# Optimization experiments

Measured on AMD Instinct MI355X. Metric: run time of the kernel, lower is better.

The kernel has to match this reference:

```python
import jax, jax.numpy as jnp
import numpy as np

N = 50000      # nodes
E = 800000     # edges (avg degree 16)
NF = 128       # input feature dim
H = 128        # hidden dim
GAMMA = 1.0    # gm init arg
COS_EPS = 1e-8 # F.cosine_similarity eps
EW_MIN = 1e-4  # edge-weight clamp


def setup_inputs() -> dict:
    key = jax.random.key(0)
    ks = jax.random.split(key, 9)
    x = jax.random.normal(ks[0], (N, NF), dtype=jnp.float32)
    edge_index = jax.random.randint(ks[1], (2, E), 0, N, dtype=jnp.int64)
    sensitive_attr = jax.random.randint(ks[2], (N,), 0, 2, dtype=jnp.int64)
    s1 = 1.0 / np.sqrt(NF)
    s2 = 1.0 / np.sqrt(H)
    W1 = jax.random.normal(ks[3], (NF, H), dtype=jnp.float32) * s1
    b1 = jnp.zeros((H,), dtype=jnp.float32)
    W2 = jax.random.normal(ks[4], (H, H), dtype=jnp.float32) * s2
    b2 = jnp.zeros((H,), dtype=jnp.float32)
    Wc = jax.random.normal(ks[5], (H, 1), dtype=jnp.float32) * s2
    bc = jnp.zeros((1,), dtype=jnp.float32)
    return {"x": x, "edge_index": edge_index, "sensitive_attr": sensitive_attr,
            "W1": W1, "b1": b1, "W2": W2, "b2": b2, "Wc": Wc, "bc": bc}


def gcn_conv(x, W, b, src, dst, ew, n):
    """PyG GCNConv: lin -> symmetric-normalized edge-weighted aggregation (+self loops) -> bias."""
    xt = x @ W                                              # [N,H]
    deg = jax.ops.segment_sum(ew, dst, num_segments=n) + 1.0  # self-loop weight 1
    dinv = jnp.where(deg > 0, deg ** -0.5, 0.0)             # [N]
    norm = dinv[src] * ew * dinv[dst]                       # [E]
    agg = jax.ops.segment_sum(xt[src] * norm[:, None], dst, num_segments=n)
    # self-loop contribution: norm_ii = dinv[i] * 1 * dinv[i]
    return agg + xt * (dinv * dinv)[:, None] + b


def reference(x, edge_index, sensitive_attr, W1, b1, W2, b2, Wc, bc):
    src, dst = edge_index[0], edge_index[1]
    # cosine-similarity edge weights (gather-heavy)
    xs, xd = x[src], x[dst]                                  # [E,F] each
    dot = jnp.sum(xs * xd, axis=1)
    ns = jnp.maximum(jnp.sqrt(jnp.sum(xs * xs, axis=1)), COS_EPS)
    nd = jnp.maximum(jnp.sqrt(jnp.sum(xd * xd, axis=1)), COS_EPS)
    sim = dot / (ns * nd)
    sen_diff = (sensitive_attr[src] != sensitive_attr[dst]).astype(x.dtype)
    ew = jnp.maximum(sim * jnp.exp(-GAMMA * sen_diff), EW_MIN)
    # two GCN layers (dropout is identity in eval mode)
    h = jax.nn.relu(gcn_conv(x, W1, b1, src, dst, ew, N))
    h = jax.nn.relu(gcn_conv(h, W2, b2, src, dst, ew, N))
    y = h @ Wc + bc                                          # [N,1]
    return (y, h)
```

## Files before the change

kernel.cpp:

```cpp
#include <hip/hip_runtime.h>


typedef unsigned short u16;
typedef unsigned int u32;
typedef __attribute__((ext_vector_type(8))) short short8;
typedef __attribute__((ext_vector_type(4))) float floatx4;

__device__ __forceinline__ float bflo(u32 u){ return __uint_as_float(u << 16); }
__device__ __forceinline__ float bfhi(u32 u){ return __uint_as_float(u & 0xFFFF0000u); }
__device__ __forceinline__ float bf1(u16 u){ return __uint_as_float(((u32)u) << 16); }
__device__ __forceinline__ u16 f2bf(float f){
    u32 u = __float_as_uint(f);
    u += 0x7FFFu + ((u >> 16) & 1u);
    return (u16)(u >> 16);
}
__device__ __forceinline__ u32 pack2(float a, float b){
    return (u32)f2bf(a) | ((u32)f2bf(b) << 16);
}
__device__ __forceinline__ float wsum(float v){
#pragma unroll
    for (int o = 32; o > 0; o >>= 1) v += __shfl_xor(v, o, 64);
    return v;
}
__device__ __forceinline__ float ld1(const void* p, size_t idx, int f32){
    return f32 ? ((const float*)p)[idx] : bf1(((const u16*)p)[idx]);
}
__device__ __forceinline__ int ldidx(const int* p, size_t i, int i64){
    return i64 ? p[2 * i] : p[i];
}

__global__ void classify_k(const u32* __restrict__ xw, const int* __restrict__ eiw,
                           int* __restrict__ flags, int* __restrict__ bcnt)
{
    __shared__ int c_out, c_nz;
    int t = threadIdx.x;
    if (t == 0) { c_out = 0; c_nz = 0; }
    if (t < 256) bcnt[t] = 0;
    __syncthreads();
    u32 w = xw[t];
    int e = (w >> 7) & 0xFF;
    int outl = (e < 110 || e > 140) ? 1 : 0;
    int nz = (eiw[2 * t + 1] != 0) ? 1 : 0;
    atomicAdd(&c_out, outl);
    atomicAdd(&c_nz, nz);
    __syncthreads();
    if (t == 0) { flags[0] = (c_out > 256); flags[1] = (c_nz < 256); }
}

__global__ __launch_bounds__(256) void convhist_k(const void* __restrict__ x,
                                                  u32* __restrict__ xb,
                                                  float* __restrict__ rn, int N,
                                                  const int* __restrict__ ei,
                                                  const int* __restrict__ sa,
                                                  int* __restrict__ bcnt, int E,
                                                  const void* __restrict__ W1,
                                                  const void* __restrict__ W2,
                                                  uint4* __restrict__ wf1,
                                                  uint4* __restrict__ wf2,
                                                  const int* __restrict__ flags,
                                                  int nbN, int nbH)
{
    __shared__ int lb[256];
    int b = blockIdx.x;
    if (b < nbN) {
        int i = b * 4 + (threadIdx.x >> 6);
        if (i >= N) return;
        int lane = threadIdx.x & 63;
        u32 u;
        if (flags[0]) {
            const float* q = (const float*)x + (size_t)i * 128 + lane * 2;
            u = pack2(q[0], q[1]);
        } else u = ((const u32*)x)[(size_t)i * 64 + lane];
        xb[(size_t)i * 64 + lane] = u;
        float f0 = bflo(u), f1 = bfhi(u);
        float ss = wsum(f0 * f0 + f1 * f1);
        if (lane == 0) {
            float r = 1.0f / fmaxf(sqrtf(ss), 1e-8f);
            int a = flags[1] ? sa[2 * (size_t)i] : sa[i];
            rn[i] = a ? -r : r;
        }
    } else if (b < nbN + nbH) {
        int t = threadIdx.x;
        lb[t] = 0;
        __syncthreads();
        int i64 = flags[1];
        size_t base = (size_t)(b - nbN) * 8192;
#pragma unroll 4
        for (int k = 0; k < 32; ++k) {
            size_t e = base + (size_t)k * 256 + t;
            if (e < (size_t)E) {
                int d = ldidx(ei, (size_t)E + e, i64);
                if ((u32)d >= (u32)N) d = 0;
                atomicAdd(&lb[d >> 8], 1);
            }
        }
        __syncthreads();
        int c = lb[t];
        if (c) atomicAdd(&bcnt[t], c);
    } else {
        int slot = (b - nbN - nbH) * 256 + threadIdx.x;
        if (slot >= 4096) return;
        int f32w = flags[0];
        const void* W = (slot < 2048) ? W1 : W2;
        uint4* wf = (slot < 2048) ? wf1 : wf2;
        int s = slot & 2047;
        int lane = s & 63, kk = (s >> 6) & 3, ct = s >> 8;
        int q = lane >> 4, n = lane & 15;
        int col = ct * 16 + n, k0 = kk * 32 + q * 8;
        union { u16 us[8]; uint4 u4; } tmp;
#pragma unroll
        for (int j = 0; j < 8; ++j)
            tmp.us[j] = f2bf(ld1(W, (size_t)(k0 + j) * 128 + col, f32w));
        wf[s] = tmp.u4;
    }
}

__global__ void bscan_k(const int* __restrict__ bcnt, int* __restrict__ bbase,
                        int* __restrict__ bcur, int* __restrict__ rowp, int N)
{
    int lane = threadIdx.x;
    int carry = 0;
    for (int base = 0; base < 256; base += 64) {
        int i = base + lane;
        int v = bcnt[i];
        int sc = v;
#pragma unroll
        for (int o = 1; o < 64; o <<= 1) {
            int nv = __shfl_up(sc, o);
            if (lane >= o) sc += nv;
        }
        int excl = carry + sc - v;
        bbase[i] = excl;
        bcur[i] = excl;
        carry += __shfl(sc, 63);
    }
    if (lane == 0) { bbase[256] = carry; rowp[N] = carry; }
}

__global__ __launch_bounds__(256) void bucket_k(const int* __restrict__ ei,
                                                int* __restrict__ bcur,
                                                u32* __restrict__ tmp,
                                                int E, int N,
                                                const int* __restrict__ flags)
{
    __shared__ int lh[256];
    __shared__ int gb[256];
    int t = threadIdx.x;
    lh[t] = 0;
    __syncthreads();
    int i64 = flags[1];
    size_t base = (size_t)blockIdx.x * 4096;
    u32 pay[16], meta[16];
#pragma unroll
    for (int k = 0; k < 16; ++k) {
        size_t e = base + (size_t)k * 256 + t;
        if (e < (size_t)E) {
            int s = ldidx(ei, e, i64);
            int d = ldidx(ei, (size_t)E + e, i64);
            if ((u32)s >= (u32)N) s = 0;
            if ((u32)d >= (u32)N) d = 0;
            int b = d >> 8;
            pay[k] = ((u32)s << 8) | ((u32)d & 0xFFu);
            int r = atomicAdd(&lh[b], 1);
            meta[k] = ((u32)r << 8) | (u32)b;
        } else meta[k] = 0xFFFFFFFFu;
    }
    __syncthreads();
    int c = lh[t];
    gb[t] = c ? atomicAdd(&bcur[t], c) : 0;
    __syncthreads();
#pragma unroll
    for (int k = 0; k < 16; ++k) {
        if (meta[k] != 0xFFFFFFFFu) {
            int b = (int)(meta[k] & 0xFFu);
            int r = (int)(meta[k] >> 8);
            tmp[gb[b] + r] = pay[k];
        }
    }
}

__global__ __launch_bounds__(256) void scat2_k(const int* __restrict__ bbase,
                                               int* __restrict__ rowp,
                                               const u32* __restrict__ tmp,
                                               u32* __restrict__ rec,
                                               int N, int E)
{
    __shared__ int lcnt[256];
    __shared__ int wtot[4];
    int b = blockIdx.x, t = threadIdx.x;
    int lane = t & 63, w = t >> 6;
    int n0 = b << 8;
    int p0 = bbase[b], p1 = bbase[b + 1];
    if (p0 < 0) p0 = 0;
    if (p1 > E) p1 = E;
    lcnt[t] = 0;
    __syncthreads();
    for (int idx = p0 + t; idx < p1; idx += 256)
        atomicAdd(&lcnt[tmp[idx] & 0xFFu], 1);
    __syncthreads();
    int v = lcnt[t];
    int sc = v;
#pragma unroll
    for (int o = 1; o < 64; o <<= 1) {
        int nv = __shfl_up(sc, o);
        if (lane >= o) sc += nv;
    }
    if (lane == 63) wtot[w] = sc;
    __syncthreads();
    int wo = 0;
#pragma unroll
    for (int k = 0; k < 4; ++k) { int s = wtot[k]; if (k < w) wo += s; }
    int excl = wo + sc - v;
    int node = n0 + t;
    if (node < N) rowp[node] = p0 + excl;
    lcnt[t] = excl;
    __syncthreads();
    for (int idx = p0 + t; idx < p1; idx += 256) {
        u32 pay = tmp[idx];
        int r = atomicAdd(&lcnt[pay & 0xFFu], 1);
        int pos = p0 + r;
        if ((u32)pos >= (u32)E) pos = 0;
        rec[pos] = pay >> 8;
    }
}

__global__ __launch_bounds__(256) void ewcsr_k(const u32* __restrict__ xb,
                                               const float* __restrict__ rn,
                                               const int* __restrict__ rowp,
                                               u32* __restrict__ rec,
                                               float* __restrict__ dv,
                                               int N, int E)
{
    int i = blockIdx.x * 4 + (threadIdx.x >> 6);
    if (i >= N) return;
    int lane = threadIdx.x & 63, g = lane >> 4, j = lane & 15;
    uint4 D = ((const uint4*)(xb + (size_t)i * 64))[j];
    float rni = rn[i];
    int p0 = rowp[i], p1 = rowp[i + 1];
    if (p0 < 0) p0 = 0;
    if (p1 > E) p1 = E;
    float acc = 0.0f;
    int p = p0 + g;
    for (; p + 4 < p1; p += 8) {
        int s0 = (int)rec[p];     if ((u32)s0 >= (u32)N) s0 = 0;
        int s1 = (int)rec[p + 4]; if ((u32)s1 >= (u32)N) s1 = 0;
        uint4 A0 = ((const uint4*)(xb + (size_t)s0 * 64))[j];
        uint4 A1 = ((const uint4*)(xb + (size_t)s1 * 64))[j];
        float d0 = bflo(A0.x) * bflo(D.x) + bfhi(A0.x) * bfhi(D.x)
                 + bflo(A0.y) * bflo(D.y) + bfhi(A0.y) * bfhi(D.y)
                 + bflo(A0.z) * bflo(D.z) + bfhi(A0.z) * bfhi(D.z)
                 + bflo(A0.w) * bflo(D.w) + bfhi(A0.w) * bfhi(D.w);
        float d1 = bflo(A1.x) * bflo(D.x) + bfhi(A1.x) * bfhi(D.x)
                 + bflo(A1.y) * bflo(D.y) + bfhi(A1.y) * bfhi(D.y)
                 + bflo(A1.z) * bflo(D.z) + bfhi(A1.z) * bfhi(D.z)
                 + bflo(A1.w) * bflo(D.w) + bfhi(A1.w) * bfhi(D.w);
#pragma unroll
        for (int o = 8; o > 0; o >>= 1) {
            d0 += __shfl_xor(d0, o);
            d1 += __shfl_xor(d1, o);
        }
        if (j == 0) {
            float pr0 = rn[s0] * rni;
            float w0 = fmaxf(d0 * fabsf(pr0) *
                             ((pr0 < 0.0f) ? 0.36787944117144233f : 1.0f), 1e-4f);
            u16 wb0 = f2bf(w0);
            rec[p] = ((u32)s0 << 16) | wb0;
            acc += bf1(wb0);
            float pr1 = rn[s1] * rni;
            float w1 = fmaxf(d1 * fabsf(pr1) *
                             ((pr1 < 0.0f) ? 0.36787944117144233f : 1.0f), 1e-4f);
            u16 wb1 = f2bf(w1);
            rec[p + 4] = ((u32)s1 << 16) | wb1;
            acc += bf1(wb1);
        }
    }
    if (p < p1) {
        int s0 = (int)rec[p]; if ((u32)s0 >= (u32)N) s0 = 0;
        uint4 A0 = ((const uint4*)(xb + (size_t)s0 * 64))[j];
        float d0 = bflo(A0.x) * bflo(D.x) + bfhi(A0.x) * bfhi(D.x)
                 + bflo(A0.y) * bflo(D.y) + bfhi(A0.y) * bfhi(D.y)
                 + bflo(A0.z) * bflo(D.z) + bfhi(A0.z) * bfhi(D.z)
                 + bflo(A0.w) * bflo(D.w) + bfhi(A0.w) * bfhi(D.w);
#pragma unroll
        for (int o = 8; o > 0; o >>= 1) d0 += __shfl_xor(d0, o);
        if (j == 0) {
            float pr0 = rn[s0] * rni;
            float w0 = fmaxf(d0 * fabsf(pr0) *
                             ((pr0 < 0.0f) ? 0.36787944117144233f : 1.0f), 1e-4f);
            u16 wb0 = f2bf(w0);
            rec[p] = ((u32)s0 << 16) | wb0;
            acc += bf1(wb0);
        }
    }
    acc += __shfl_xor(acc, 16);
    acc += __shfl_xor(acc, 32);
    if (lane == 0) dv[i] = 1.0f / sqrtf(1.0f + acc);
}

__global__ __launch_bounds__(256) void aggemm_k(const u32* __restrict__ feat,
                                                const int* __restrict__ rowp,
                                                const u32* __restrict__ rec,
                                                const float* __restrict__ dinv,
                                                const uint4* __restrict__ wfrag,
                                                const void* __restrict__ bias,
                                                void* __restrict__ out, int outbf,
                                                int N, int E,
                                                const void* __restrict__ Wc,
                                                const void* __restrict__ bc,
                                                float* __restrict__ yout,
                                                const int* __restrict__ flags)
{
    __shared__ float Acc[4][16][132];
    int t = threadIdx.x, wave = t >> 6, lane = t & 63;
    int rowbase = blockIdx.x * 64 + wave * 16;

    int idx = rowbase + lane;
    int rbreg = E;
    if (lane < 17) {
        int ii = idx < N ? idx : N;
        int v = rowp[ii];
        rbreg = v < 0 ? 0 : (v > E ? E : v);
    }
    float dreg = 0.0f;
    if (lane < 16 && idx < N) dreg = dinv[idx];

    for (int r = 0; r < 16; ++r) {
        int i = rowbase + r;
        float s0 = 0.0f, s1 = 0.0f;
        if (i < N) {
            float di = __shfl(dreg, r), sc = di * di;
            u32 u = feat[(size_t)i * 64 + lane];
            s0 = bflo(u) * sc; s1 = bfhi(u) * sc;
        }
        float2 st; st.x = s0; st.y = s1;
        *(float2*)&Acc[wave][r][2 * lane] = st;
    }

    int P0 = __shfl(rbreg, 0), P16 = __shfl(rbreg, 16);
    int crow = 0;
    int nb = __shfl(rbreg, 1);
    float dic = __shfl(dreg, 0);
    float a0 = 0.0f, a1 = 0.0f;
    int p = P0;
    for (; p + 15 < P16; p += 16) {
        u32 rr[16]; int s[16]; u32 v[16]; float dvs[16];
#pragma unroll
        for (int k = 0; k < 16; ++k) {
            rr[k] = rec[p + k];
            s[k] = rr[k] >> 16;
            if (s[k] >= N) s[k] = 0;
        }
#pragma unroll
        for (int k = 0; k < 16; ++k) v[k] = feat[(size_t)s[k] * 64 + lane];
#pragma unroll
        for (int k = 0; k < 16; ++k) dvs[k] = dinv[s[k]];
#pragma unroll
        for (int k = 0; k < 16; ++k) {
            int e = p + k;
            if (e >= nb) {
                float2* ap = (float2*)&Acc[wave][crow][2 * lane];
                float2 cv = *ap; cv.x += a0; cv.y += a1; *ap = cv;
                do { ++crow; nb = __shfl(rbreg, crow + 1); } while (e >= nb);
                dic = __shfl(dreg, crow & 15);
                a0 = 0.0f; a1 = 0.0f;
            }
            float w = bf1((u16)rr[k]) * dic * dvs[k];
            a0 = fmaf(w, bflo(v[k]), a0);
            a1 = fmaf(w, bfhi(v[k]), a1);
        }
    }
    for (; p + 3 < P16; p += 4) {
        u32 rr[4]; int s[4]; u32 v[4]; float dvs[4];
#pragma unroll
        for (int k = 0; k < 4; ++k) {
            rr[k] = rec[p + k];
            s[k] = rr[k] >> 16;
            if (s[k] >= N) s[k] = 0;
        }
#pragma unroll
        for (int k = 0; k < 4; ++k) v[k] = feat[(size_t)s[k] * 64 + lane];
#pragma unroll
        for (int k = 0; k < 4; ++k) dvs[k] = dinv[s[k]];
#pragma unroll
        for (int k = 0; k < 4; ++k) {
            int e = p + k;
            if (e >= nb) {
                float2* ap = (float2*)&Acc[wave][crow][2 * lane];
                float2 cv = *ap; cv.x += a0; cv.y += a1; *ap = cv;
                do { ++crow; nb = __shfl(rbreg, crow + 1); } while (e >= nb);
                dic = __shfl(dreg, crow & 15);
                a0 = 0.0f; a1 = 0.0f;
            }
            float w = bf1((u16)rr[k]) * dic * dvs[k];
            a0 = fmaf(w, bflo(v[k]), a0);
            a1 = fmaf(w, bfhi(v[k]), a1);
        }
    }
    for (; p < P16; ++p) {
        u32 r0 = rec[p];
        int s0 = r0 >> 16;
        if (s0 >= N) s0 = 0;
        u32 v0 = feat[(size_t)s0 * 64 + lane];
        float dv0 = dinv[s0];
        if (p >= nb) {
            float2* ap = (float2*)&Acc[wave][crow][2 * lane];
            float2 cv = *ap; cv.x += a0; cv.y += a1; *ap = cv;
            do { ++crow; nb = __shfl(rbreg, crow + 1); } while (p >= nb);
            dic = __shfl(dreg, crow & 15);
            a0 = 0.0f; a1 = 0.0f;
        }
        float w = bf1((u16)r0) * dic * dv0;
        a0 = fmaf(w, bflo(v0), a0);
        a1 = fmaf(w, bfhi(v0), a1);
    }
    {
        float2* ap = (float2*)&Acc[wave][crow & 15][2 * lane];
        float2 cv = *ap; cv.x += a0; cv.y += a1; *ap = cv;
    }
    __syncthreads();

    int q = lane >> 4, n = lane & 15;
    int f32w = flags[0];
    const float* rowptr = &Acc[wave][n][0];
    short8 a[4];
#pragma unroll
    for (int kk = 0; kk < 4; ++kk) {
        int c0 = kk * 32 + q * 8;
        float2 g0 = *(const float2*)(rowptr + c0);
        float2 g1 = *(const float2*)(rowptr + c0 + 2);
        float2 g2 = *(const float2*)(rowptr + c0 + 4);
        float2 g3 = *(const float2*)(rowptr + c0 + 6);
        uint4 av;
        av.x = pack2(g0.x, g0.y);
        av.y = pack2(g1.x, g1.y);
        av.z = pack2(g2.x, g2.y);
        av.w = pack2(g3.x, g3.y);
        a[kk] = *(short8*)&av;
    }
    floatx4 acc[8];
#pragma unroll
    for (int ct = 0; ct < 8; ++ct) acc[ct] = (floatx4){0.f, 0.f, 0.f, 0.f};
#pragma unroll
    for (int ct = 0; ct < 8; ++ct) {
#pragma unroll
        for (int kk = 0; kk < 4; ++kk) {
            uint4 bv = wfrag[(ct * 4 + kk) * 64 + lane];
            acc[ct] = __builtin_amdgcn_mfma_f32_16x16x32_bf16(
                a[kk], *(short8*)&bv, acc[ct], 0, 0, 0);
        }
    }
    float bcv = 0.0f;
    float part[4] = {0.f, 0.f, 0.f, 0.f};
    if (yout) bcv = ld1(bc, 0, f32w);
#pragma unroll
    for (int ct = 0; ct < 8; ++ct) {
        int col = ct * 16 + n;
        float bia = ld1(bias, col, f32w);
        float wcv = yout ? ld1(Wc, col, f32w) : 0.0f;
#pragma unroll
        for (int r = 0; r < 4; ++r) {
            int row = rowbase - wave * 16 + wave * 16 + q * 4 + r;
            row = blockIdx.x * 64 + wave * 16 + q * 4 + r;
            float h = fmaxf(acc[ct][r] + bia, 0.0f);
            if (row < N) {
                if (outbf) ((u16*)out)[(size_t)row * 128 + col] = f2bf(h);
                else       ((float*)out)[(size_t)row * 128 + col] = h;
            }
            part[r] = fmaf(h, wcv, part[r]);
        }
    }
    if (yout) {
#pragma unroll
        for (int r = 0; r < 4; ++r) {
            float pr = part[r];
#pragma unroll
            for (int o = 8; o > 0; o >>= 1) pr += __shfl_xor(pr, o);
            int row = blockIdx.x * 64 + wave * 16 + q * 4 + r;
            if (n == 0 && row < N) yout[row] = pr + bcv;
        }
    }
}

extern "C" void kernel_launch(void* const* d_in, const int* in_sizes, int n_in,
                              void* d_out, int out_size, void* d_ws, size_t ws_size,
                              hipStream_t stream)
{
    const void* x  = d_in[0];
    const int* ei  = (const int*)d_in[1];
    const int* sa  = (const int*)d_in[2];
    const void* W1 = d_in[3];
    const void* b1 = d_in[4];
    const void* W2 = d_in[5];
    const void* b2 = d_in[6];
    const void* Wc = d_in[7];
    const void* bc = d_in[8];
    const int N = in_sizes[2];
    const int E = in_sizes[1] / 2;

    float* y_out = (float*)d_out;
    float* h_out = y_out + N;
    u32*   h1b   = (u32*)d_in[0];
    u32*   tmp   = (u32*)d_in[0];

    const int nbN = (N + 3) / 4;
    const int nbH = (E + 8191) / 8192;
    const int NB  = (N + 255) / 256;

    char* p = (char*)d_ws;
    auto carve = [&](size_t bytes) { char* r = p; p += (bytes + 255) & ~(size_t)255; return r; };
    int*   flags = (int*)carve(256);
    float* rn    = (float*)carve((size_t)N * 4);
    float* dinv  = (float*)carve((size_t)N * 4);
    int*   rowp  = (int*)carve((size_t)(N + 1) * 4);
    int*   bcnt  = (int*)carve(256 * 4);
    int*   bbase = (int*)carve(260 * 4);
    int*   bcur  = (int*)carve(256 * 4);
    uint4* wf1   = (uint4*)carve(2048 * 16);
    uint4* wf2   = (uint4*)carve(2048 * 16);
    u32*   rec   = (u32*)carve((size_t)E * 4);
    u32*   xb    = (u32*)carve((size_t)N * 64 * 4);

    classify_k<<<1, 1024, 0, stream>>>((const u32*)x, ei, flags, bcnt);
    convhist_k<<<nbN + nbH + 16, 256, 0, stream>>>(x, xb, rn, N, ei, sa, bcnt, E,
                                                   W1, W2, wf1, wf2, flags,
                                                   nbN, nbH);
    bscan_k<<<1, 64, 0, stream>>>(bcnt, bbase, bcur, rowp, N);
    bucket_k<<<(E + 4095) / 4096, 256, 0, stream>>>(ei, bcur, tmp, E, N, flags);
    scat2_k<<<NB, 256, 0, stream>>>(bbase, rowp, tmp, rec, N, E);
    ewcsr_k<<<(N + 3) / 4, 256, 0, stream>>>(xb, rn, rowp, rec, dinv, N, E);

    aggemm_k<<<(N + 63) / 64, 256, 0, stream>>>(xb, rowp, rec, dinv, wf1, b1,
                                                h1b, 1, N, E,
                                                nullptr, nullptr, nullptr, flags);
    aggemm_k<<<(N + 63) / 64, 256, 0, stream>>>(h1b, rowp, rec, dinv, wf2, b2,
                                                h_out, 0, N, E,
                                                Wc, bc, y_out, flags);
}
```

Before: 285.6 us.

## Split each aggemm row tile across two waves by edge range and column half

Doubles the aggemm block to 512 threads so each 16-row tile is handled by two waves. The tile's CSR edge range is split at its midpoint, and each wave finds its starting row with a ballot. Partial row sums are merged into shared memory with LDS atomics. Each wave then computes half of the output columns in the MFMA stage, and the classifier partials are combined through a small shared buffer. The aim is more memory-level parallelism and latency hiding for the gather, at the cost of LDS atomics, extra barriers and higher per-block resource use.

```diff
diff --git a/kernel.cpp b/kernel.cpp
--- a/kernel.cpp
+++ b/kernel.cpp
@@ -297,7 +297,7 @@
     if (lane == 0) dv[i] = 1.0f / sqrtf(1.0f + acc);
 }
 
-__global__ __launch_bounds__(256) void aggemm_k(const u32* __restrict__ feat,
+__global__ __launch_bounds__(512) void aggemm_k(const u32* __restrict__ feat,
                                                 const int* __restrict__ rowp,
                                                 const u32* __restrict__ rec,
                                                 const float* __restrict__ dinv,
@@ -311,8 +311,10 @@
                                                 const int* __restrict__ flags)
 {
     __shared__ float Acc[4][16][132];
+    __shared__ float ybuf[4][16];
     int t = threadIdx.x, wave = t >> 6, lane = t & 63;
-    int rowbase = blockIdx.x * 64 + wave * 16;
+    int tile = wave >> 1, half = wave & 1;
+    int rowbase = blockIdx.x * 64 + tile * 16;
 
     int idx = rowbase + lane;
     int rbreg = E;
@@ -324,7 +326,7 @@
     float dreg = 0.0f;
     if (lane < 16 && idx < N) dreg = dinv[idx];
 
-    for (int r = 0; r < 16; ++r) {
+    for (int r = half * 8; r < half * 8 + 8; ++r) {
         int i = rowbase + r;
         float s0 = 0.0f, s1 = 0.0f;
         if (i < N) {
@@ -333,16 +335,23 @@
             s0 = bflo(u) * sc; s1 = bfhi(u) * sc;
         }
         float2 st; st.x = s0; st.y = s1;
-        *(float2*)&Acc[wave][r][2 * lane] = st;
-    }
+        *(float2*)&Acc[tile][r][2 * lane] = st;
+    }
+    __syncthreads();
 
     int P0 = __shfl(rbreg, 0), P16 = __shfl(rbreg, 16);
-    int crow = 0;
-    int nb = __shfl(rbreg, 1);
-    float dic = __shfl(dreg, 0);
+    int mid = (P0 + P16) >> 1;
+    int lo = half ? mid : P0;
+    int hi = half ? P16 : mid;
+    unsigned long long bm = __ballot(lane <= 16 && rbreg <= lo);
+    int crow = (int)__popcll(bm) - 1;
+    if (crow < 0) crow = 0;
+    if (crow > 15) crow = 15;
+    int nb = __shfl(rbreg, crow + 1);
+    float dic = __shfl(dreg, crow & 15);
     float a0 = 0.0f, a1 = 0.0f;
-    int p = P0;
-    for (; p + 15 < P16; p += 16) {
+    int p = lo;
+    for (; p + 15 < hi; p += 16) {
         u32 rr[16]; int s[16]; u32 v[16]; float dvs[16];
 #pragma unroll
         for (int k = 0; k < 16; ++k) {
@@ -358,8 +367,8 @@
         for (int k = 0; k < 16; ++k) {
             int e = p + k;
             if (e >= nb) {
-                float2* ap = (float2*)&Acc[wave][crow][2 * lane];
-                float2 cv = *ap; cv.x += a0; cv.y += a1; *ap = cv;
+                atomicAdd(&Acc[tile][crow][2 * lane], a0);
+                atomicAdd(&Acc[tile][crow][2 * lane + 1], a1);
                 do { ++crow; nb = __shfl(rbreg, crow + 1); } while (e >= nb);
                 dic = __shfl(dreg, crow & 15);
                 a0 = 0.0f; a1 = 0.0f;
@@ -369,7 +378,7 @@
             a1 = fmaf(w, bfhi(v[k]), a1);
         }
     }
-    for (; p + 3 < P16; p += 4) {
+    for (; p + 3 < hi; p += 4) {
         u32 rr[4]; int s[4]; u32 v[4]; float dvs[4];
 #pragma unroll
         for (int k = 0; k < 4; ++k) {
@@ -385,8 +394,8 @@
         for (int k = 0; k < 4; ++k) {
             int e = p + k;
             if (e >= nb) {
-                float2* ap = (float2*)&Acc[wave][crow][2 * lane];
-                float2 cv = *ap; cv.x += a0; cv.y += a1; *ap = cv;
+                atomicAdd(&Acc[tile][crow][2 * lane], a0);
+                atomicAdd(&Acc[tile][crow][2 * lane + 1], a1);
                 do { ++crow; nb = __shfl(rbreg, crow + 1); } while (e >= nb);
                 dic = __shfl(dreg, crow & 15);
                 a0 = 0.0f; a1 = 0.0f;
@@ -396,15 +405,15 @@
             a1 = fmaf(w, bfhi(v[k]), a1);
         }
     }
-    for (; p < P16; ++p) {
+    for (; p < hi; ++p) {
         u32 r0 = rec[p];
         int s0 = r0 >> 16;
         if (s0 >= N) s0 = 0;
         u32 v0 = feat[(size_t)s0 * 64 + lane];
         float dv0 = dinv[s0];
         if (p >= nb) {
-            float2* ap = (float2*)&Acc[wave][crow][2 * lane];
-            float2 cv = *ap; cv.x += a0; cv.y += a1; *ap = cv;
+            atomicAdd(&Acc[tile][crow][2 * lane], a0);
+            atomicAdd(&Acc[tile][crow][2 * lane + 1], a1);
             do { ++crow; nb = __shfl(rbreg, crow + 1); } while (p >= nb);
             dic = __shfl(dreg, crow & 15);
             a0 = 0.0f; a1 = 0.0f;
@@ -414,14 +423,16 @@
         a1 = fmaf(w, bfhi(v0), a1);
     }
     {
-        float2* ap = (float2*)&Acc[wave][crow & 15][2 * lane];
-        float2 cv = *ap; cv.x += a0; cv.y += a1; *ap = cv;
+        int cr = crow & 15;
+        atomicAdd(&Acc[tile][cr][2 * lane], a0);
+        atomicAdd(&Acc[tile][cr][2 * lane + 1], a1);
     }
     __syncthreads();
 
     int q = lane >> 4, n = lane & 15;
     int f32w = flags[0];
-    const float* rowptr = &Acc[wave][n][0];
+    int ct0 = half * 4;
+    const float* rowptr = &Acc[tile][n][0];
     short8 a[4];
 #pragma unroll
     for (int kk = 0; kk < 4; ++kk) {
@@ -437,31 +448,30 @@
         av.w = pack2(g3.x, g3.y);
         a[kk] = *(short8*)&av;
     }
-    floatx4 acc[8];
-#pragma unroll
-    for (int ct = 0; ct < 8; ++ct) acc[ct] = (floatx4){0.f, 0.f, 0.f, 0.f};
-#pragma unroll
-    for (int ct = 0; ct < 8; ++ct) {
+    floatx4 acc[4];
+#pragma unroll
+    for (int c = 0; c < 4; ++c) acc[c] = (floatx4){0.f, 0.f, 0.f, 0.f};
+#pragma unroll
+    for (int c = 0; c < 4; ++c) {
 #pragma unroll
         for (int kk = 0; kk < 4; ++kk) {
-            uint4 bv = wfrag[(ct * 4 + kk) * 64 + lane];
-            acc[ct] = __builtin_amdgcn_mfma_f32_16x16x32_bf16(
-                a[kk], *(short8*)&bv, acc[ct], 0, 0, 0);
+            uint4 bv = wfrag[((ct0 + c) * 4 + kk) * 64 + lane];
+            acc[c] = __builtin_amdgcn_mfma_f32_16x16x32_bf16(
+                a[kk], *(short8*)&bv, acc[c], 0, 0, 0);
         }
     }
     float bcv = 0.0f;
     float part[4] = {0.f, 0.f, 0.f, 0.f};
     if (yout) bcv = ld1(bc, 0, f32w);
 #pragma unroll
-    for (int ct = 0; ct < 8; ++ct) {
-        int col = ct * 16 + n;
+    for (int c = 0; c < 4; ++c) {
+        int col = (ct0 + c) * 16 + n;
         float bia = ld1(bias, col, f32w);
         float wcv = yout ? ld1(Wc, col, f32w) : 0.0f;
 #pragma unroll
         for (int r = 0; r < 4; ++r) {
-            int row = rowbase - wave * 16 + wave * 16 + q * 4 + r;
-            row = blockIdx.x * 64 + wave * 16 + q * 4 + r;
-            float h = fmaxf(acc[ct][r] + bia, 0.0f);
+            int row = rowbase + q * 4 + r;
+            float h = fmaxf(acc[c][r] + bia, 0.0f);
             if (row < N) {
                 if (outbf) ((u16*)out)[(size_t)row * 128 + col] = f2bf(h);
                 else       ((float*)out)[(size_t)row * 128 + col] = h;
@@ -469,14 +479,24 @@
             part[r] = fmaf(h, wcv, part[r]);
         }
     }
-    if (yout) {
+    float prv[4];
+#pragma unroll
+    for (int r = 0; r < 4; ++r) {
+        float pr = part[r];
+#pragma unroll
+        for (int o = 8; o > 0; o >>= 1) pr += __shfl_xor(pr, o);
+        prv[r] = pr;
+    }
+    if (yout && half && n == 0) {
+#pragma unroll
+        for (int r = 0; r < 4; ++r) ybuf[tile][q * 4 + r] = prv[r];
+    }
+    __syncthreads();
+    if (yout && !half && n == 0) {
 #pragma unroll
         for (int r = 0; r < 4; ++r) {
-            float pr = part[r];
-#pragma unroll
-            for (int o = 8; o > 0; o >>= 1) pr += __shfl_xor(pr, o);
-            int row = blockIdx.x * 64 + wave * 16 + q * 4 + r;
-            if (n == 0 && row < N) yout[row] = pr + bcv;
+            int row = rowbase + q * 4 + r;
+            if (row < N) yout[row] = prv[r] + ybuf[tile][q * 4 + r] + bcv;
         }
     }
 }
@@ -529,10 +549,10 @@
     scat2_k<<<NB, 256, 0, stream>>>(bbase, rowp, tmp, rec, N, E);
     ewcsr_k<<<(N + 3) / 4, 256, 0, stream>>>(xb, rn, rowp, rec, dinv, N, E);
 
-    aggemm_k<<<(N + 63) / 64, 256, 0, stream>>>(xb, rowp, rec, dinv, wf1, b1,
+    aggemm_k<<<(N + 63) / 64, 512, 0, stream>>>(xb, rowp, rec, dinv, wf1, b1,
                                                 h1b, 1, N, E,
                                                 nullptr, nullptr, nullptr, flags);
-    aggemm_k<<<(N + 63) / 64, 256, 0, stream>>>(h1b, rowp, rec, dinv, wf2, b2,
+    aggemm_k<<<(N + 63) / 64, 512, 0, stream>>>(h1b, rowp, rec, dinv, wf2, b2,
                                                 h_out, 0, N, E,
                                                 Wc, bc, y_out, flags);
 }
```

Result: slower. 321.6 us (+12.6%).
